# Kernel tuning notes

Measured on AMD Instinct MI355X. Metric: run time of the kernel, lower is better.

The kernel has to match this reference:

```python
import jax, jax.numpy as jnp
import numpy as np

UNITS = 256
GROUPS = 8
EPS = 1e-3  # keras GroupNormalization default epsilon


def group_norm(x, gamma, beta, groups=GROUPS, eps=EPS):
    # x: [B,H,W,C], normalize per group over (H,W,C//groups)
    B, H, W, C = x.shape
    xg = x.reshape(B, H, W, groups, C // groups)
    mean = xg.mean(axis=(1, 2, 4), keepdims=True)
    var = xg.var(axis=(1, 2, 4), keepdims=True)
    xn = (xg - mean) * jax.lax.rsqrt(var + eps)
    xn = xn.reshape(B, H, W, C)
    return xn * gamma + beta


def setup_inputs() -> dict:
    key = jax.random.key(0)
    ks = jax.random.split(key, 10)
    B, H, W, C = 4, 64, 64, UNITS
    s = 1.0 / np.sqrt(C)
    x = jax.random.normal(ks[0], (B, H, W, C), dtype=jnp.float32)
    return {
        "x": x,
        "gamma": jnp.ones((C,), jnp.float32),
        "beta": jnp.zeros((C,), jnp.float32),
        "Wq": jax.random.uniform(ks[1], (C, C), jnp.float32, -s, s),
        "bq": jnp.zeros((C,), jnp.float32),
        "Wk": jax.random.uniform(ks[2], (C, C), jnp.float32, -s, s),
        "bk": jnp.zeros((C,), jnp.float32),
        "Wv": jax.random.uniform(ks[3], (C, C), jnp.float32, -s, s),
        "bv": jnp.zeros((C,), jnp.float32),
        # proj kernel init scale ~0 -> near-zero weights; use tiny random for nontrivial grads
        "Wp": jax.random.uniform(ks[4], (C, C), jnp.float32, -1e-5, 1e-5),
        "bp": jnp.zeros((C,), jnp.float32),
    }


def reference(x, gamma, beta, Wq, bq, Wk, bk, Wv, bv, Wp, bp):
    B, H, W, C = x.shape
    scale = jnp.float32(C) ** -0.5
    xn = group_norm(x, gamma, beta)  # [B,H,W,C]
    n = H * W
    xf = xn.reshape(B, n, C)
    q = xf @ Wq + bq  # [B,N,C]
    k = xf @ Wk + bk
    v = xf @ Wv + bv
    attn = jnp.einsum('bnc,bmc->bnm', q, k) * scale  # [B,N,N]
    attn = jax.nn.softmax(attn, axis=-1)
    out = jnp.einsum('bnm,bmc->bnc', attn, v)  # [B,N,C]
    out = out @ Wp + bp
    # NOTE: original code reassigns `inputs = self.norm(inputs)` before the
    # residual, so the skip connection uses the NORMALIZED input.
    return xn + out.reshape(B, H, W, C)
```

## Files before the change

### kernel.cpp

```cpp
#include <hip/hip_runtime.h>
#include <hip/hip_bf16.h>

typedef unsigned short u16;
typedef unsigned char u8;
typedef short short8 __attribute__((ext_vector_type(8)));
typedef float floatx4 __attribute__((ext_vector_type(4)));
typedef long long i64;

#define BB 4
#define NN 4096
#define CC 256
#define NG 8
#define M_TOT (BB * NN)
#define GN_EPS 1e-3f
#define ATT_SCALE 0.0625f
#define MCONST 2.5f

__device__ __forceinline__ u16 f2bf(float f) {
  __hip_bfloat16 h = __float2bfloat16(f);
  return __builtin_bit_cast(u16, h);
}
__device__ __forceinline__ float bf2f(u16 u) {
  unsigned int i = ((unsigned int)u) << 16;
  return __builtin_bit_cast(float, i);
}
__device__ __forceinline__ unsigned pack2(float a, float b) {
  return (unsigned)f2bf(a) | ((unsigned)f2bf(b) << 16);
}
__device__ __forceinline__ unsigned pk4f8(float a, float b, float c, float d) {
  unsigned v = __builtin_amdgcn_cvt_pk_fp8_f32(a, b, 0, false);
  v = __builtin_amdgcn_cvt_pk_fp8_f32(c, d, v, true);
  return v;
}
__device__ __forceinline__ u8 f8byte(float a) {
  return (u8)(__builtin_amdgcn_cvt_pk_fp8_f32(a, a, 0, false) & 0xFF);
}

typedef __attribute__((address_space(3))) unsigned int lds_u32;
typedef const __attribute__((address_space(1))) unsigned int glb_u32;
#define ASYNC16(g, l) \
  __builtin_amdgcn_global_load_lds((glb_u32*)(g), (lds_u32*)(l), 16, 0, 0)

__global__ void prep_stats(const float* __restrict__ x,
                           const float* __restrict__ Wq, const float* __restrict__ Wk,
                           const float* __restrict__ Wv, const float* __restrict__ Wp,
                           float* __restrict__ part,
                           u16* __restrict__ wqT, u16* __restrict__ wkT,
                           u16* __restrict__ wvT, u16* __restrict__ wpT) {
  __shared__ u16 Ts[64][68];
  int blk = blockIdx.x;
  int t = threadIdx.x;
  if (blk < 512) {
    int b = blk >> 7, chunk = blk & 127;
    const float* p = x + ((size_t)b * NN + chunk * 32) * CC + t;
    float s = 0.f, ss = 0.f;
    for (int i = 0; i < 32; ++i) { float v = p[(size_t)i * CC]; s += v; ss += v * v; }
    for (int off = 1; off < 32; off <<= 1) { s += __shfl_xor(s, off); ss += __shfl_xor(ss, off); }
    if ((t & 31) == 0) {
      int g = t >> 5;
      part[((size_t)blk * NG + g) * 2 + 0] = s;
      part[((size_t)blk * NG + g) * 2 + 1] = ss;
    }
  } else {
    int pid = blk - 512;
    int y = pid >> 4, tile = pid & 15;
    int o0 = (tile >> 2) * 64, c0 = (tile & 3) * 64;
    const float* W = (y == 0) ? Wq : (y == 1) ? Wk : (y == 2) ? Wv : Wp;
    u16* WT = (y == 0) ? wqT : (y == 1) ? wkT : (y == 2) ? wvT : wpT;
    int cl = t >> 4, o4 = t & 15;
    for (int it = 0; it < 4; ++it) {
      int c = cl + it * 16;
      float4 v = *reinterpret_cast<const float4*>(W + (size_t)(c0 + c) * CC + o0 + o4 * 4);
      Ts[c][o4 * 4 + 0] = f2bf(v.x); Ts[c][o4 * 4 + 1] = f2bf(v.y);
      Ts[c][o4 * 4 + 2] = f2bf(v.z); Ts[c][o4 * 4 + 3] = f2bf(v.w);
    }
    __syncthreads();
    int ol = t >> 3, c8 = t & 7;
    for (int it = 0; it < 2; ++it) {
      int o = ol + it * 32;
      uint4 uv;
      uv.x = (unsigned)Ts[c8 * 8 + 0][o] | ((unsigned)Ts[c8 * 8 + 1][o] << 16);
      uv.y = (unsigned)Ts[c8 * 8 + 2][o] | ((unsigned)Ts[c8 * 8 + 3][o] << 16);
      uv.z = (unsigned)Ts[c8 * 8 + 4][o] | ((unsigned)Ts[c8 * 8 + 5][o] << 16);
      uv.w = (unsigned)Ts[c8 * 8 + 6][o] | ((unsigned)Ts[c8 * 8 + 7][o] << 16);
      *reinterpret_cast<uint4*>(WT + (size_t)(o0 + o) * CC + c0 + c8 * 8) = uv;
    }
  }
}

__global__ __launch_bounds__(256) void gn_apply(
    const float* __restrict__ x, const float* __restrict__ gamma,
    const float* __restrict__ beta, const float* __restrict__ part,
    u16* __restrict__ xnb) {
  __shared__ float gnst[16];
  int blk = blockIdx.x;
  int t = threadIdx.x;
  int b = blk >> 7;
  if (t < 64) {
    int g = t >> 3, j = t & 7;
    float s = 0.f, ss = 0.f;
    for (int ch = j; ch < 128; ch += 8) {
      size_t idx = (((size_t)(b * 128 + ch)) * NG + g) * 2;
      s += part[idx]; ss += part[idx + 1];
    }
    for (int off = 1; off < 8; off <<= 1) { s += __shfl_xor(s, off); ss += __shfl_xor(ss, off); }
    if (j == 0) {
      const float cnt = (float)(NN * (CC / NG));
      float mean = s / cnt;
      float var = ss / cnt - mean * mean;
      gnst[g * 2] = mean;
      gnst[g * 2 + 1] = rsqrtf(var + GN_EPS);
    }
  }
  __syncthreads();
  int row0 = blk * 32;
#pragma unroll
  for (int it = 0; it < 8; ++it) {
    int idx = t + it * 256;
    int rl = idx >> 6, c4 = idx & 63;
    int g = c4 >> 3;
    float mean = gnst[g * 2], rstd = gnst[g * 2 + 1];
    size_t gidx = (size_t)(row0 + rl) * 64 + c4;
    float4 v = reinterpret_cast<const float4*>(x)[gidx];
    float4 gm = reinterpret_cast<const float4*>(gamma)[c4];
    float4 bt = reinterpret_cast<const float4*>(beta)[c4];
    ushort4 o;
    o.x = f2bf((v.x - mean) * rstd * gm.x + bt.x);
    o.y = f2bf((v.y - mean) * rstd * gm.y + bt.y);
    o.z = f2bf((v.z - mean) * rstd * gm.z + bt.z);
    o.w = f2bf((v.w - mean) * rstd * gm.w + bt.w);
    reinterpret_cast<ushort4*>(xnb)[gidx] = o;
  }
}

#define LDT 72
__global__ __launch_bounds__(256) void gemm_qkv(
    const u16* __restrict__ xnb,
    const u16* __restrict__ wqT, const u16* __restrict__ wkT, const u16* __restrict__ wvT,
    const float* __restrict__ bq, const float* __restrict__ bk, const float* __restrict__ bv,
    u8* __restrict__ qb, u8* __restrict__ kb, u8* __restrict__ vTb) {
  __shared__ u16 sm[2 * 128 * LDT];
  u16* Asp = sm;
  u16* Bsp = sm + 128 * LDT;
  int m0 = blockIdx.x * 128;
  int widx = blockIdx.y >> 1;
  int n0 = (blockIdx.y & 1) * 128;
  const u16* wT = (widx == 0) ? wqT : (widx == 1) ? wkT : wvT;
  const float* bias = (widx == 0) ? bq : (widx == 1) ? bk : bv;
  int t = threadIdx.x, w = t >> 6, lane = t & 63, lo = lane & 15, hi = lane >> 4;
  int wm = (w >> 1) * 64, wn = (w & 1) * 64;
  floatx4 acc[4][4];
  for (int i = 0; i < 4; ++i) for (int j = 0; j < 4; ++j) acc[i][j] = (floatx4){0.f, 0.f, 0.f, 0.f};
  for (int kt = 0; kt < 4; ++kt) {
    int k0 = kt * 64;
    __syncthreads();
    for (int i = 0; i < 4; ++i) {
      int idx = t + i * 256, r = idx >> 3, c8 = idx & 7;
      *reinterpret_cast<uint4*>(Asp + r * LDT + c8 * 8) =
          *reinterpret_cast<const uint4*>(xnb + (size_t)(m0 + r) * CC + k0 + c8 * 8);
      *reinterpret_cast<uint4*>(Bsp + r * LDT + c8 * 8) =
          *reinterpret_cast<const uint4*>(wT + (size_t)(n0 + r) * CC + k0 + c8 * 8);
    }
    __syncthreads();
    for (int k32 = 0; k32 < 2; ++k32) {
      short8 af[4], bfr[4];
      for (int mt = 0; mt < 4; ++mt)
        af[mt] = *reinterpret_cast<const short8*>(Asp + (wm + mt * 16 + lo) * LDT + k32 * 32 + hi * 8);
      for (int nt = 0; nt < 4; ++nt)
        bfr[nt] = *reinterpret_cast<const short8*>(Bsp + (wn + nt * 16 + lo) * LDT + k32 * 32 + hi * 8);
      for (int mt = 0; mt < 4; ++mt)
        for (int nt = 0; nt < 4; ++nt)
          acc[mt][nt] = __builtin_amdgcn_mfma_f32_16x16x32_bf16(af[mt], bfr[nt], acc[mt][nt], 0, 0, 0);
    }
  }
  __syncthreads();
  for (int mt = 0; mt < 4; ++mt)
    for (int nt = 0; nt < 4; ++nt)
      for (int r = 0; r < 4; ++r) {
        int rr = wm + mt * 16 + hi * 4 + r;
        int cc2 = wn + nt * 16 + lo;
        sm[rr * 130 + cc2] = f2bf(acc[mt][nt][r] + bias[n0 + cc2]);
      }
  __syncthreads();
  if (widx < 2) {
    u8* outp = (widx == 0) ? qb : kb;
    for (int j = 0; j < 8; ++j) {
      int c = t + j * 256;
      int row = c >> 4, chl = c & 15;
      const u16* sp = sm + row * 130 + chl * 8;
      uint2 val;
      val.x = pk4f8(bf2f(sp[0]), bf2f(sp[1]), bf2f(sp[2]), bf2f(sp[3]));
      val.y = pk4f8(bf2f(sp[4]), bf2f(sp[5]), bf2f(sp[6]), bf2f(sp[7]));
      int rowg = m0 + row;
      int chg = (n0 >> 3) + chl;
      int chs = (widx == 0) ? chg : ((chg + 2 * (rowg & 15)) & 31);
      *reinterpret_cast<uint2*>(outp + (size_t)rowg * CC + chs * 8) = val;
    }
  } else {
    for (int ss = 0; ss < 2; ++ss) {
      int seg = t + ss * 256;
      int dloc = seg & 127, tt = seg >> 7;
      int dglob = n0 + dloc;
      int rot = (dglob >> 1) & 3;
      uint2 arr[4];
      for (int g = 0; g < 4; ++g) {
        int base = tt * 32 + 4 * g;
        unsigned w0 = pk4f8(bf2f(sm[(base + 0) * 130 + dloc]), bf2f(sm[(base + 1) * 130 + dloc]),
                            bf2f(sm[(base + 2) * 130 + dloc]), bf2f(sm[(base + 3) * 130 + dloc]));
        unsigned w1 = pk4f8(bf2f(sm[(base + 16) * 130 + dloc]), bf2f(sm[(base + 17) * 130 + dloc]),
                            bf2f(sm[(base + 18) * 130 + dloc]), bf2f(sm[(base + 19) * 130 + dloc]));
        arr[(g + rot) & 3] = (uint2){w0, w1};
      }
      int tokg = m0 + tt * 32;
      int bb = tokg >> 12, tk = tokg & (NN - 1);
      u8* dst = vTb + ((size_t)(bb * CC + dglob)) * NN + tk;
      *reinterpret_cast<uint4*>(dst) = (uint4){arr[0].x, arr[0].y, arr[1].x, arr[1].y};
      *reinterpret_cast<uint4*>(dst + 16) = (uint4){arr[2].x, arr[2].y, arr[3].x, arr[3].y};
    }
  }
}

__global__ __launch_bounds__(256, 2) void fa_kernel(
    const u8* __restrict__ qb, const u8* __restrict__ kb, const u8* __restrict__ vTb,
    u8* __restrict__ Opart, float* __restrict__ Lpart, u16* __restrict__ aob, int S) {
  __shared__ u8 Ks[32 * 256];
  __shared__ u8 vTs[256 * 32];
  int by = blockIdx.y;
  int b = by / S, split = by - b * S;
  int t = threadIdx.x, w = t >> 6, lane = t & 63, lo = lane & 15, hi = lane >> 4;
  int qw = blockIdx.x * 128 + w * 32;

  i64 qf[2][8];
#pragma unroll
  for (int qg = 0; qg < 2; ++qg) {
    const u8* qrow = qb + ((size_t)(b * NN + qw + qg * 16 + lo)) * CC;
#pragma unroll
    for (int ds = 0; ds < 8; ++ds)
      qf[qg][ds] = *reinterpret_cast<const i64*>(qrow + ds * 32 + hi * 8);
  }
  floatx4 oacc[2][16];
#pragma unroll
  for (int qg = 0; qg < 2; ++qg)
#pragma unroll
    for (int dt = 0; dt < 16; ++dt) oacc[qg][dt] = (floatx4){0.f, 0.f, 0.f, 0.f};
  float lacc[2] = {0.f, 0.f};

  const int TILES = NN / 32;
  int jt0 = split * (TILES / S), jt1 = jt0 + TILES / S;
  const u8* kb_b = kb + (size_t)b * NN * CC;
  const u8* vb_b = vTb + (size_t)b * CC * NN;

  for (int jt = jt0; jt < jt1; ++jt) {
    int j0 = jt * 32;
    __syncthreads();
    {
      const u8* gk = kb_b + (size_t)j0 * CC;
#pragma unroll
      for (int rnd = 0; rnd < 2; ++rnd) {
        int o = (w * 2 + rnd) * 1024;
        ASYNC16(gk + o + lane * 16, Ks + o);
      }
#pragma unroll
      for (int rnd = 0; rnd < 2; ++rnd) {
        int o = (w * 2 + rnd) * 1024;
        int o16 = o + lane * 16;
        const u8* gv = vb_b + (size_t)(o16 >> 5) * NN + j0 + (o16 & 31);
        ASYNC16(gv, vTs + o);
      }
    }
    __syncthreads();

    floatx4 s[2][2];
#pragma unroll
    for (int qg = 0; qg < 2; ++qg)
#pragma unroll
      for (int st = 0; st < 2; ++st) s[qg][st] = (floatx4){0.f, 0.f, 0.f, 0.f};
#pragma unroll
    for (int ds = 0; ds < 8; ++ds) {
      int ch = ds * 4 + hi;
      int pch = (ch + 2 * lo) & 31;
      i64 k0 = *reinterpret_cast<const i64*>(Ks + lo * 256 + pch * 8);
      i64 k1 = *reinterpret_cast<const i64*>(Ks + (16 + lo) * 256 + pch * 8);
#pragma unroll
      for (int qg = 0; qg < 2; ++qg) {
        s[qg][0] = __builtin_amdgcn_mfma_f32_16x16x32_fp8_fp8(k0, qf[qg][ds], s[qg][0], 0, 0, 0);
        s[qg][1] = __builtin_amdgcn_mfma_f32_16x16x32_fp8_fp8(k1, qf[qg][ds], s[qg][1], 0, 0, 0);
      }
    }
    i64 pA[2];
#pragma unroll
    for (int qg = 0; qg < 2; ++qg) {
      float p0 = __expf(fmaf(s[qg][0][0], ATT_SCALE, -MCONST));
      float p1 = __expf(fmaf(s[qg][0][1], ATT_SCALE, -MCONST));
      float p2 = __expf(fmaf(s[qg][0][2], ATT_SCALE, -MCONST));
      float p3 = __expf(fmaf(s[qg][0][3], ATT_SCALE, -MCONST));
      float p4 = __expf(fmaf(s[qg][1][0], ATT_SCALE, -MCONST));
      float p5 = __expf(fmaf(s[qg][1][1], ATT_SCALE, -MCONST));
      float p6 = __expf(fmaf(s[qg][1][2], ATT_SCALE, -MCONST));
      float p7 = __expf(fmaf(s[qg][1][3], ATT_SCALE, -MCONST));
      lacc[qg] += (p0 + p1 + p2 + p3) + (p4 + p5 + p6 + p7);
      uint2 uu;
      uu.x = pk4f8(p0, p1, p2, p3);
      uu.y = pk4f8(p4, p5, p6, p7);
      pA[qg] = __builtin_bit_cast(i64, uu);
    }
#pragma unroll
    for (int dt = 0; dt < 16; ++dt) {
      int d = dt * 16 + lo;
      int gp = (hi + ((d >> 1) & 3)) & 3;
      i64 vf = *reinterpret_cast<const i64*>(vTs + d * 32 + gp * 8);
      oacc[0][dt] = __builtin_amdgcn_mfma_f32_16x16x32_fp8_fp8(pA[0], vf, oacc[0][dt], 0, 0, 0);
      oacc[1][dt] = __builtin_amdgcn_mfma_f32_16x16x32_fp8_fp8(pA[1], vf, oacc[1][dt], 0, 0, 0);
    }
  }

#pragma unroll
  for (int qg = 0; qg < 2; ++qg) {
    lacc[qg] += __shfl_xor(lacc[qg], 16);
    lacc[qg] += __shfl_xor(lacc[qg], 32);
  }

  if (S == 1) {
#pragma unroll
    for (int qg = 0; qg < 2; ++qg) {
      float inv[4];
#pragma unroll
      for (int r = 0; r < 4; ++r) inv[r] = 1.0f / __shfl(lacc[qg], 4 * hi + r);
#pragma unroll
      for (int dt = 0; dt < 16; ++dt)
#pragma unroll
        for (int r = 0; r < 4; ++r) {
          size_t row = (size_t)(b * NN + qw + qg * 16 + 4 * hi + r);
          aob[row * CC + dt * 16 + lo] = f2bf(oacc[qg][dt][r] * inv[r]);
        }
    }
  } else {
    if (hi == 0) {
#pragma unroll
      for (int qg = 0; qg < 2; ++qg)
        Lpart[(size_t)split * M_TOT + b * NN + qw + qg * 16 + lo] = lacc[qg];
    }
    u8* op = Opart + (size_t)split * M_TOT * CC;
#pragma unroll
    for (int qg = 0; qg < 2; ++qg)
#pragma unroll
      for (int dt = 0; dt < 16; ++dt)
#pragma unroll
        for (int r = 0; r < 4; ++r) {
          size_t row = (size_t)(b * NN + qw + qg * 16 + 4 * hi + r);
          op[row * CC + dt * 16 + lo] = f8byte(oacc[qg][dt][r]);
        }
  }
}

__global__ __launch_bounds__(256) void gemm_proj(
    const u16* __restrict__ aob, const u8* __restrict__ Opart,
    const float* __restrict__ Lpart,
    const u16* __restrict__ wpT, const float* __restrict__ bp,
    const u16* __restrict__ xnb, float* __restrict__ out, int S) {
  __shared__ u16 As[64 * LDT];
  __shared__ u16 Bs[128 * LDT];
  __shared__ float linv[64];
  int m0 = blockIdx.x * 64;
  int n0 = blockIdx.y * 128;
  int t = threadIdx.x, w = t >> 6, lane = t & 63, lo = lane & 15, hi = lane >> 4;
  int wm = (w >> 1) * 32, wn = (w & 1) * 64;
  if (S > 1 && t < 64) {
    float l = 0.f;
    for (int sp = 0; sp < S; ++sp) l += Lpart[(size_t)sp * M_TOT + m0 + t];
    linv[t] = 1.f / l;
  }
  floatx4 acc[2][4];
  for (int i = 0; i < 2; ++i) for (int j = 0; j < 4; ++j) acc[i][j] = (floatx4){0.f, 0.f, 0.f, 0.f};
  for (int kt = 0; kt < 4; ++kt) {
    int k0 = kt * 64;
    __syncthreads();
    for (int i = 0; i < 2; ++i) {
      int c = t + i * 256, r = c >> 3, c8 = c & 7;
      if (S == 1) {
        *reinterpret_cast<uint4*>(As + r * LDT + c8 * 8) =
            *reinterpret_cast<const uint4*>(aob + (size_t)(m0 + r) * CC + k0 + c8 * 8);
      } else {
        float f[8] = {0, 0, 0, 0, 0, 0, 0, 0};
        for (int sp = 0; sp < S; ++sp) {
          uint2 uv = *reinterpret_cast<const uint2*>(
              Opart + (size_t)sp * M_TOT * CC + (size_t)(m0 + r) * CC + k0 + c8 * 8);
          f[0] += __builtin_amdgcn_cvt_f32_fp8(uv.x, 0);
          f[1] += __builtin_amdgcn_cvt_f32_fp8(uv.x, 1);
          f[2] += __builtin_amdgcn_cvt_f32_fp8(uv.x, 2);
          f[3] += __builtin_amdgcn_cvt_f32_fp8(uv.x, 3);
          f[4] += __builtin_amdgcn_cvt_f32_fp8(uv.y, 0);
          f[5] += __builtin_amdgcn_cvt_f32_fp8(uv.y, 1);
          f[6] += __builtin_amdgcn_cvt_f32_fp8(uv.y, 2);
          f[7] += __builtin_amdgcn_cvt_f32_fp8(uv.y, 3);
        }
        float iv = linv[r];
        uint4 o;
        o.x = pack2(f[0] * iv, f[1] * iv); o.y = pack2(f[2] * iv, f[3] * iv);
        o.z = pack2(f[4] * iv, f[5] * iv); o.w = pack2(f[6] * iv, f[7] * iv);
        *reinterpret_cast<uint4*>(As + r * LDT + c8 * 8) = o;
      }
    }
    for (int i = 0; i < 4; ++i) {
      int c = t + i * 256, r = c >> 3, c8 = c & 7;
      *reinterpret_cast<uint4*>(Bs + r * LDT + c8 * 8) =
          *reinterpret_cast<const uint4*>(wpT + (size_t)(n0 + r) * CC + k0 + c8 * 8);
    }
    __syncthreads();
    for (int k32 = 0; k32 < 2; ++k32) {
      short8 af[2], bfr[4];
      for (int mt = 0; mt < 2; ++mt)
        af[mt] = *reinterpret_cast<const short8*>(As + (wm + mt * 16 + lo) * LDT + k32 * 32 + hi * 8);
      for (int nt = 0; nt < 4; ++nt)
        bfr[nt] = *reinterpret_cast<const short8*>(Bs + (wn + nt * 16 + lo) * LDT + k32 * 32 + hi * 8);
      for (int mt = 0; mt < 2; ++mt)
        for (int nt = 0; nt < 4; ++nt)
          acc[mt][nt] = __builtin_amdgcn_mfma_f32_16x16x32_bf16(af[mt], bfr[nt], acc[mt][nt], 0, 0, 0);
    }
  }
  for (int mt = 0; mt < 2; ++mt)
    for (int nt = 0; nt < 4; ++nt)
      for (int r = 0; r < 4; ++r) {
        int row = m0 + wm + mt * 16 + hi * 4 + r;
        int col = n0 + wn + nt * 16 + lo;
        size_t o = (size_t)row * CC + col;
        out[o] = acc[mt][nt][r] + bp[col] + bf2f(xnb[o]);
      }
}

extern "C" void kernel_launch(void* const* d_in, const int* in_sizes, int n_in,
                              void* d_out, int out_size, void* d_ws, size_t ws_size,
                              hipStream_t stream) {
  (void)in_sizes; (void)n_in; (void)out_size;
  const float* x     = (const float*)d_in[0];
  const float* gamma = (const float*)d_in[1];
  const float* beta  = (const float*)d_in[2];
  const float* Wq    = (const float*)d_in[3];
  const float* bq    = (const float*)d_in[4];
  const float* Wk    = (const float*)d_in[5];
  const float* bk    = (const float*)d_in[6];
  const float* Wv    = (const float*)d_in[7];
  const float* bv    = (const float*)d_in[8];
  const float* Wp    = (const float*)d_in[9];
  const float* bp    = (const float*)d_in[10];
  float* out = (float*)d_out;

  char* w = (char*)d_ws;
  float* part  = (float*)w;              w += 512 * NG * 2 * 4;
  const size_t SZ = (size_t)M_TOT * CC * 2;
  const size_t SZ8 = (size_t)M_TOT * CC;
  u16* xnb = (u16*)w; w += SZ;
  u8* qb   = (u8*)w;  w += SZ8;
  u8* kb   = (u8*)w;  w += SZ8;
  u8* vTb  = (u8*)w;  w += SZ8;
  u16* aob = (u16*)w; w += SZ;
  u16* wqT = (u16*)w; w += (size_t)CC * CC * 2;
  u16* wkT = (u16*)w; w += (size_t)CC * CC * 2;
  u16* wvT = (u16*)w; w += (size_t)CC * CC * 2;
  u16* wpT = (u16*)w; w += (size_t)CC * CC * 2;

  size_t used = (size_t)(w - (char*)d_ws);
  size_t per_split = SZ8 + (size_t)M_TOT * 4 + 256;
  int S = 4;
  if (used + 4 * per_split > ws_size) S = 2;
  if (used + 2 * per_split > ws_size) S = 1;
  u8* Opart = (u8*)w;                    w += (size_t)S * SZ8;
  float* Lpart = (float*)w;

  prep_stats<<<576, 256, 0, stream>>>(x, Wq, Wk, Wv, Wp, part, wqT, wkT, wvT, wpT);
  gn_apply<<<512, 256, 0, stream>>>(x, gamma, beta, part, xnb);
  gemm_qkv<<<dim3(M_TOT / 128, 6), 256, 0, stream>>>(xnb, wqT, wkT, wvT, bq, bk, bv, qb, kb, vTb);
  fa_kernel<<<dim3(NN / 128, BB * S), 256, 0, stream>>>(qb, kb, vTb, Opart, Lpart, aob, S);
  gemm_proj<<<dim3(M_TOT / 64, 2), 256, 0, stream>>>(aob, Opart, Lpart, wpT, bp, xnb, out, S);
}
```

Measured before the change: 196.3 us.

## Use 16x16x128 scaled FP8 MFMA with 128-key tiles and XOR-swizzled LDS

Replaces the 16x16x32 FP8 MFMA in the attention kernel with the MI355X mfma_scale 16x16x128 f8f6f4 instruction using unit scales. The key tile grows from 32 to 128 keys per iteration, and shared-memory layouts switch to XOR swizzles for K and V^T. The QKV epilogue drops its old rotation swizzles and writes V^T in the token order the new P operand expects. The aim is fewer MFMA issues and fewer loop-iteration barriers. In exchange, shared memory grows from 16KB to 64KB per block, which can reduce occupancy below the two blocks per CU that the launch bounds request.

Result: slower. 246.6 us (+25.6%).

```diff
diff --git a/kernel.cpp b/kernel.cpp
--- a/kernel.cpp
+++ b/kernel.cpp
@@ -5,6 +5,7 @@
 typedef unsigned char u8;
 typedef short short8 __attribute__((ext_vector_type(8)));
 typedef float floatx4 __attribute__((ext_vector_type(4)));
+typedef int intx8 __attribute__((ext_vector_type(8)));
 typedef long long i64;
 
 #define BB 4
@@ -15,6 +16,7 @@
 #define GN_EPS 1e-3f
 #define ATT_SCALE 0.0625f
 #define MCONST 2.5f
+#define UNIT_SCALE 0x7F7F7F7F
 
 __device__ __forceinline__ u16 f2bf(float f) {
   __hip_bfloat16 h = __float2bfloat16(f);
@@ -193,29 +195,30 @@
       val.y = pk4f8(bf2f(sp[4]), bf2f(sp[5]), bf2f(sp[6]), bf2f(sp[7]));
       int rowg = m0 + row;
       int chg = (n0 >> 3) + chl;
-      int chs = (widx == 0) ? chg : ((chg + 2 * (rowg & 15)) & 31);
-      *reinterpret_cast<uint2*>(outp + (size_t)rowg * CC + chs * 8) = val;
+      *reinterpret_cast<uint2*>(outp + (size_t)rowg * CC + chg * 8) = val;
     }
   } else {
-    for (int ss = 0; ss < 2; ++ss) {
-      int seg = t + ss * 256;
-      int dloc = seg & 127, tt = seg >> 7;
-      int dglob = n0 + dloc;
-      int rot = (dglob >> 1) & 3;
-      uint2 arr[4];
-      for (int g = 0; g < 4; ++g) {
-        int base = tt * 32 + 4 * g;
-        unsigned w0 = pk4f8(bf2f(sm[(base + 0) * 130 + dloc]), bf2f(sm[(base + 1) * 130 + dloc]),
-                            bf2f(sm[(base + 2) * 130 + dloc]), bf2f(sm[(base + 3) * 130 + dloc]));
-        unsigned w1 = pk4f8(bf2f(sm[(base + 16) * 130 + dloc]), bf2f(sm[(base + 17) * 130 + dloc]),
-                            bf2f(sm[(base + 18) * 130 + dloc]), bf2f(sm[(base + 19) * 130 + dloc]));
-        arr[(g + rot) & 3] = (uint2){w0, w1};
-      }
-      int tokg = m0 + tt * 32;
-      int bb = tokg >> 12, tk = tokg & (NN - 1);
-      u8* dst = vTb + ((size_t)(bb * CC + dglob)) * NN + tk;
-      *reinterpret_cast<uint4*>(dst) = (uint4){arr[0].x, arr[0].y, arr[1].x, arr[1].y};
-      *reinterpret_cast<uint4*>(dst + 16) = (uint4){arr[2].x, arr[2].y, arr[3].x, arr[3].y};
+    int dloc = t & 127;
+    int dglob = n0 + dloc;
+    int bb = m0 >> 12, tk = m0 & (NN - 1);
+    u8* dst = vTb + ((size_t)(bb * CC + dglob)) * NN + tk;
+#pragma unroll
+    for (int it = 0; it < 2; ++it) {
+      int ub = (t >> 7) * 2 + it * 4;
+      unsigned wds[8];
+#pragma unroll
+      for (int uo = 0; uo < 2; ++uo) {
+        int u = ub + uo;
+        int rbase = 64 * (u & 1) + 4 * (u >> 1);
+#pragma unroll
+        for (int q = 0; q < 4; ++q) {
+          int r0 = rbase + q * 16;
+          wds[uo * 4 + q] = pk4f8(bf2f(sm[(r0 + 0) * 130 + dloc]), bf2f(sm[(r0 + 1) * 130 + dloc]),
+                                  bf2f(sm[(r0 + 2) * 130 + dloc]), bf2f(sm[(r0 + 3) * 130 + dloc]));
+        }
+      }
+      *reinterpret_cast<uint4*>(dst + ub * 16) = (uint4){wds[0], wds[1], wds[2], wds[3]};
+      *reinterpret_cast<uint4*>(dst + ub * 16 + 16) = (uint4){wds[4], wds[5], wds[6], wds[7]};
     }
   }
 }
@@ -223,20 +226,24 @@
 __global__ __launch_bounds__(256, 2) void fa_kernel(
     const u8* __restrict__ qb, const u8* __restrict__ kb, const u8* __restrict__ vTb,
     u8* __restrict__ Opart, float* __restrict__ Lpart, u16* __restrict__ aob, int S) {
-  __shared__ u8 Ks[32 * 256];
-  __shared__ u8 vTs[256 * 32];
+  __shared__ u8 Ks[128 * 256];
+  __shared__ u8 vTs[256 * 128];
   int by = blockIdx.y;
   int b = by / S, split = by - b * S;
   int t = threadIdx.x, w = t >> 6, lane = t & 63, lo = lane & 15, hi = lane >> 4;
   int qw = blockIdx.x * 128 + w * 32;
 
-  i64 qf[2][8];
+  intx8 qf[2][2];
 #pragma unroll
   for (int qg = 0; qg < 2; ++qg) {
     const u8* qrow = qb + ((size_t)(b * NN + qw + qg * 16 + lo)) * CC;
 #pragma unroll
-    for (int ds = 0; ds < 8; ++ds)
-      qf[qg][ds] = *reinterpret_cast<const i64*>(qrow + ds * 32 + hi * 8);
+    for (int kk = 0; kk < 2; ++kk) {
+      uint4 a0 = *reinterpret_cast<const uint4*>(qrow + kk * 128 + hi * 32);
+      uint4 a1 = *reinterpret_cast<const uint4*>(qrow + kk * 128 + hi * 32 + 16);
+      qf[qg][kk] = (intx8){(int)a0.x, (int)a0.y, (int)a0.z, (int)a0.w,
+                           (int)a1.x, (int)a1.y, (int)a1.z, (int)a1.w};
+    }
   }
   floatx4 oacc[2][16];
 #pragma unroll
@@ -245,72 +252,79 @@
     for (int dt = 0; dt < 16; ++dt) oacc[qg][dt] = (floatx4){0.f, 0.f, 0.f, 0.f};
   float lacc[2] = {0.f, 0.f};
 
-  const int TILES = NN / 32;
+  const int TILES = NN / 128;
   int jt0 = split * (TILES / S), jt1 = jt0 + TILES / S;
   const u8* kb_b = kb + (size_t)b * NN * CC;
   const u8* vb_b = vTb + (size_t)b * CC * NN;
 
   for (int jt = jt0; jt < jt1; ++jt) {
-    int j0 = jt * 32;
-    __syncthreads();
-    {
-      const u8* gk = kb_b + (size_t)j0 * CC;
-#pragma unroll
-      for (int rnd = 0; rnd < 2; ++rnd) {
-        int o = (w * 2 + rnd) * 1024;
-        ASYNC16(gk + o + lane * 16, Ks + o);
-      }
-#pragma unroll
-      for (int rnd = 0; rnd < 2; ++rnd) {
-        int o = (w * 2 + rnd) * 1024;
-        int o16 = o + lane * 16;
-        const u8* gv = vb_b + (size_t)(o16 >> 5) * NN + j0 + (o16 & 31);
-        ASYNC16(gv, vTs + o);
-      }
-    }
-    __syncthreads();
-
-    floatx4 s[2][2];
-#pragma unroll
-    for (int qg = 0; qg < 2; ++qg)
-#pragma unroll
-      for (int st = 0; st < 2; ++st) s[qg][st] = (floatx4){0.f, 0.f, 0.f, 0.f};
-#pragma unroll
-    for (int ds = 0; ds < 8; ++ds) {
-      int ch = ds * 4 + hi;
-      int pch = (ch + 2 * lo) & 31;
-      i64 k0 = *reinterpret_cast<const i64*>(Ks + lo * 256 + pch * 8);
-      i64 k1 = *reinterpret_cast<const i64*>(Ks + (16 + lo) * 256 + pch * 8);
+    int j0 = jt * 128;
+    __syncthreads();
+#pragma unroll
+    for (int i = 0; i < 8; ++i) {
+      int base = w * 512 + i * 64;
+      int sl = base + lane;
+      int row = sl >> 4;
+      int u = (sl & 15) ^ (row & 7);
+      ASYNC16(kb_b + (size_t)(j0 + row) * CC + u * 16, Ks + base * 16);
+    }
+#pragma unroll
+    for (int i = 0; i < 8; ++i) {
+      int base = w * 512 + i * 64;
+      int sl = base + lane;
+      int d = sl >> 3;
+      int u = (sl & 7) ^ (d & 7);
+      ASYNC16(vb_b + (size_t)d * NN + j0 + u * 16, vTs + base * 16);
+    }
+    __syncthreads();
+
+    int pAw[2][8];
+#pragma unroll
+    for (int g = 0; g < 8; ++g) {
+      int row = g * 16 + lo;
+      const u8* kr = Ks + row * 256;
+      int rs = row & 7;
+      intx8 kf[2];
+#pragma unroll
+      for (int kk = 0; kk < 2; ++kk) {
+        uint4 c0 = *reinterpret_cast<const uint4*>(kr + ((kk * 8 + hi * 2 + 0) ^ rs) * 16);
+        uint4 c1 = *reinterpret_cast<const uint4*>(kr + ((kk * 8 + hi * 2 + 1) ^ rs) * 16);
+        kf[kk] = (intx8){(int)c0.x, (int)c0.y, (int)c0.z, (int)c0.w,
+                         (int)c1.x, (int)c1.y, (int)c1.z, (int)c1.w};
+      }
 #pragma unroll
       for (int qg = 0; qg < 2; ++qg) {
-        s[qg][0] = __builtin_amdgcn_mfma_f32_16x16x32_fp8_fp8(k0, qf[qg][ds], s[qg][0], 0, 0, 0);
-        s[qg][1] = __builtin_amdgcn_mfma_f32_16x16x32_fp8_fp8(k1, qf[qg][ds], s[qg][1], 0, 0, 0);
-      }
-    }
-    i64 pA[2];
-#pragma unroll
-    for (int qg = 0; qg < 2; ++qg) {
-      float p0 = __expf(fmaf(s[qg][0][0], ATT_SCALE, -MCONST));
-      float p1 = __expf(fmaf(s[qg][0][1], ATT_SCALE, -MCONST));
-      float p2 = __expf(fmaf(s[qg][0][2], ATT_SCALE, -MCONST));
-      float p3 = __expf(fmaf(s[qg][0][3], ATT_SCALE, -MCONST));
-      float p4 = __expf(fmaf(s[qg][1][0], ATT_SCALE, -MCONST));
-      float p5 = __expf(fmaf(s[qg][1][1], ATT_SCALE, -MCONST));
-      float p6 = __expf(fmaf(s[qg][1][2], ATT_SCALE, -MCONST));
-      float p7 = __expf(fmaf(s[qg][1][3], ATT_SCALE, -MCONST));
-      lacc[qg] += (p0 + p1 + p2 + p3) + (p4 + p5 + p6 + p7);
-      uint2 uu;
-      uu.x = pk4f8(p0, p1, p2, p3);
-      uu.y = pk4f8(p4, p5, p6, p7);
-      pA[qg] = __builtin_bit_cast(i64, uu);
-    }
+        floatx4 s = (floatx4){0.f, 0.f, 0.f, 0.f};
+        s = __builtin_amdgcn_mfma_scale_f32_16x16x128_f8f6f4(
+            kf[0], qf[qg][0], s, 0, 0, 0, UNIT_SCALE, 0, UNIT_SCALE);
+        s = __builtin_amdgcn_mfma_scale_f32_16x16x128_f8f6f4(
+            kf[1], qf[qg][1], s, 0, 0, 0, UNIT_SCALE, 0, UNIT_SCALE);
+        float p0 = __expf(fmaf(s[0], ATT_SCALE, -MCONST));
+        float p1 = __expf(fmaf(s[1], ATT_SCALE, -MCONST));
+        float p2 = __expf(fmaf(s[2], ATT_SCALE, -MCONST));
+        float p3 = __expf(fmaf(s[3], ATT_SCALE, -MCONST));
+        lacc[qg] += (p0 + p1) + (p2 + p3);
+        pAw[qg][g] = (int)pk4f8(p0, p1, p2, p3);
+      }
+    }
+    intx8 pA0 = (intx8){pAw[0][0], pAw[0][1], pAw[0][2], pAw[0][3],
+                        pAw[0][4], pAw[0][5], pAw[0][6], pAw[0][7]};
+    intx8 pA1 = (intx8){pAw[1][0], pAw[1][1], pAw[1][2], pAw[1][3],
+                        pAw[1][4], pAw[1][5], pAw[1][6], pAw[1][7]};
+
 #pragma unroll
     for (int dt = 0; dt < 16; ++dt) {
       int d = dt * 16 + lo;
-      int gp = (hi + ((d >> 1) & 3)) & 3;
-      i64 vf = *reinterpret_cast<const i64*>(vTs + d * 32 + gp * 8);
-      oacc[0][dt] = __builtin_amdgcn_mfma_f32_16x16x32_fp8_fp8(pA[0], vf, oacc[0][dt], 0, 0, 0);
-      oacc[1][dt] = __builtin_amdgcn_mfma_f32_16x16x32_fp8_fp8(pA[1], vf, oacc[1][dt], 0, 0, 0);
+      const u8* vr = vTs + d * 128;
+      int ds7 = d & 7;
+      uint4 v0 = *reinterpret_cast<const uint4*>(vr + ((hi * 2 + 0) ^ ds7) * 16);
+      uint4 v1 = *reinterpret_cast<const uint4*>(vr + ((hi * 2 + 1) ^ ds7) * 16);
+      intx8 vf = (intx8){(int)v0.x, (int)v0.y, (int)v0.z, (int)v0.w,
+                         (int)v1.x, (int)v1.y, (int)v1.z, (int)v1.w};
+      oacc[0][dt] = __builtin_amdgcn_mfma_scale_f32_16x16x128_f8f6f4(
+          pA0, vf, oacc[0][dt], 0, 0, 0, UNIT_SCALE, 0, UNIT_SCALE);
+      oacc[1][dt] = __builtin_amdgcn_mfma_scale_f32_16x16x128_f8f6f4(
+          pA1, vf, oacc[1][dt], 0, 0, 0, UNIT_SCALE, 0, UNIT_SCALE);
     }
   }
 
```
